# Kernel optimization log

Measured on AMD Instinct MI355X. Metric: run time of the kernel, lower is better.

## Reference

```python
import jax, jax.numpy as jnp
import numpy as np

B, S, D, H, HD = 4, 2048, 2048, 16, 128
NEG_INF = -1e10


def setup_inputs() -> dict:
    key = jax.random.key(0)
    ks = jax.random.split(key, 7)
    scale = 1.0 / np.sqrt(D)  # variance_scaling(1.0, 'fan_in') approx
    inputs_q = jax.random.normal(ks[0], (B, S, D), jnp.float32)
    inputs_kv = jax.random.normal(ks[1], (B, S, D), jnp.float32)
    mask = jax.random.randint(ks[2], (B, 1, S, S), 0, 2, jnp.int32)
    Wq = jax.random.normal(ks[3], (D, H, HD), jnp.float32) * scale
    Wk = jax.random.normal(ks[4], (D, H, HD), jnp.float32) * scale
    Wv = jax.random.normal(ks[5], (D, H, HD), jnp.float32) * scale
    Wo = jax.random.normal(ks[6], (H, HD, D), jnp.float32) * (1.0 / np.sqrt(H * HD))
    return {"inputs_q": inputs_q, "inputs_kv": inputs_kv, "mask": mask,
            "Wq": Wq, "Wk": Wk, "Wv": Wv, "Wo": Wo}


def reference(inputs_q, inputs_kv, mask, Wq, Wk, Wv, Wo):
    # QKV projections: [B,S,D] x [D,H,HD] -> [B,S,H,HD]
    q = jnp.einsum('bsd,dhk->bshk', inputs_q, Wq)
    k = jnp.einsum('bsd,dhk->bshk', inputs_kv, Wk)
    v = jnp.einsum('bsd,dhk->bshk', inputs_kv, Wv)
    # mask -> additive bias: 0 where mask>0, else -1e10
    attn_bias = jnp.where(mask > 0, 0.0, NEG_INF).astype(q.dtype)  # [B,1,S,S]
    # scaled dot-product attention
    q = q / jnp.sqrt(jnp.asarray(HD, q.dtype))
    logits = jnp.einsum('bqhd,bkhd->bhqk', q, k) + attn_bias  # [B,H,S,S]
    weights = jax.nn.softmax(logits, axis=-1)
    x = jnp.einsum('bhqk,bkhd->bqhd', weights, v)  # [B,S,H,HD]
    # out projection contracts (heads, head_dim) -> embed
    out = jnp.einsum('bqhd,hdo->bqo', x, Wo)  # [B,S,D]
    return out
```

## Files before the change

kernel.cpp:

```cpp
#include <hip/hip_runtime.h>

typedef __attribute__((ext_vector_type(4))) float f32x4;
typedef __attribute__((ext_vector_type(8))) short bf16x8;
typedef unsigned int uint;
typedef unsigned short ushort;


__device__ __forceinline__ ushort f2bf(float f) {
  union { float f; uint u; } v; v.f = f;
  uint u = v.u;
  uint r = (u + 0x7FFFu + ((u >> 16) & 1u)) >> 16;
  return (ushort)r;
}
__device__ __forceinline__ float to_f32(float f) { return f; }
__device__ __forceinline__ float to_f32(ushort u) {
  union { uint u; float f; } v; v.u = ((uint)u) << 16;
  return v.f;
}

__device__ __forceinline__ uint cvt_pk_bf16(float lo, float hi) {
  uint r;
  asm("v_cvt_pk_bf16_f32 %0, %1, %2" : "=v"(r) : "v"(lo), "v"(hi));
  return r;
}

__device__ __forceinline__ void gload_lds16(const void* g, void* l) {
  __builtin_amdgcn_global_load_lds(
      (const __attribute__((address_space(1))) void*)g,
      (__attribute__((address_space(3))) void*)l, 16, 0, 0);
}


__global__ __launch_bounds__(256)
void conv_bf16(const float* __restrict__ in, ushort* __restrict__ out, long n) {
  long i = ((long)blockIdx.x * 256 + threadIdx.x) * 8;
  if (i >= n) return;
  float4 a = *(const float4*)(in + i);
  float4 b = *(const float4*)(in + i + 4);
  union { ushort u[8]; uint4 v; } o;
  o.u[0] = f2bf(a.x); o.u[1] = f2bf(a.y); o.u[2] = f2bf(a.z); o.u[3] = f2bf(a.w);
  o.u[4] = f2bf(b.x); o.u[5] = f2bf(b.y); o.u[6] = f2bf(b.z); o.u[7] = f2bf(b.w);
  *(uint4*)(out + i) = o.v;
}

template<typename T>
__global__ __launch_bounds__(256)
void transpose_to_bf16(const T* __restrict__ in, ushort* __restrict__ out, int R, int C) {
  __shared__ float tile[32][33];
  const size_t boff = (size_t)blockIdx.z * R * C;
  in += boff; out += boff;
  const int r0 = blockIdx.y * 32, c0 = blockIdx.x * 32;
  const int x = threadIdx.x, y = threadIdx.y;
#pragma unroll
  for (int j = 0; j < 32; j += 8)
    tile[y + j][x] = to_f32(in[(size_t)(r0 + y + j) * C + c0 + x]);
  __syncthreads();
#pragma unroll
  for (int j = 0; j < 32; j += 8)
    out[(size_t)(c0 + y + j) * R + r0 + x] = f2bf(tile[x][y + j]);
}

__global__ __launch_bounds__(256)
void pack_mask(const int* __restrict__ in, uint* __restrict__ out) {
  long t = (long)blockIdx.x * 256 + threadIdx.x;
  const int4* p = (const int4*)(in + t * 32);
  uint w = 0;
#pragma unroll
  for (int i = 0; i < 8; ++i) {
    int4 v = p[i];
    w |= (v.x > 0 ? 1u : 0u) << (i * 4 + 0);
    w |= (v.y > 0 ? 1u : 0u) << (i * 4 + 1);
    w |= (v.z > 0 ? 1u : 0u) << (i * 4 + 2);
    w |= (v.w > 0 ? 1u : 0u) << (i * 4 + 3);
  }
  out[t] = w;
}


template<int OUT_BF16>
__global__ __launch_bounds__(512, 2)
void gemm256(const ushort* __restrict__ A, const ushort* __restrict__ Bt,
             void* __restrict__ C, int M, int N, int K, float scale) {
  __shared__ ushort lA[2][256 * 64];
  __shared__ ushort lB[2][256 * 64];
  const int tid = threadIdx.x;
  const int wid = tid >> 6, lane = tid & 63;
  const int lg = lane >> 4, li = lane & 15;
  const int wm = wid >> 2, wn = wid & 3;
  const int m0 = blockIdx.y * 256, n0 = blockIdx.x * 256;

  int offA[4], offB[4];
#pragma unroll
  for (int i = 0; i < 4; ++i) {
    int off = i * 8192 + tid * 16;
    int row = off >> 7;
    int col = (off & 127) ^ ((row & 7) << 4);
    offA[i] = (m0 + row) * (K * 2) + col;
    offB[i] = (n0 + row) * (K * 2) + col;
  }
  const char* Ab = (const char*)A;
  const char* Bb = (const char*)Bt;

#define STAGE256(bufi, ktb)                                                   \
  do {                                                                        \
    _Pragma("unroll") for (int i = 0; i < 4; ++i)                             \
      gload_lds16(Ab + (size_t)(offA[i] + (ktb)),                             \
                  (char*)lA[bufi] + i * 8192 + wid * 1024);                   \
    _Pragma("unroll") for (int i = 0; i < 4; ++i)                             \
      gload_lds16(Bb + (size_t)(offB[i] + (ktb)),                             \
                  (char*)lB[bufi] + i * 8192 + wid * 1024);                   \
  } while (0)

  f32x4 acc[8][4] = {};
  const int NT = K >> 6;

  STAGE256(0, 0);

  for (int t = 0; t < NT; ++t) {
    const int cur = t & 1;
    if (t > 0) __builtin_amdgcn_s_barrier();
    if (t + 1 < NT) {
      STAGE256(cur ^ 1, (t + 1) * 128);
      asm volatile("s_waitcnt vmcnt(8)" ::: "memory");
    } else {
      asm volatile("s_waitcnt vmcnt(0)" ::: "memory");
    }
    __builtin_amdgcn_s_barrier();
    __builtin_amdgcn_sched_barrier(0);

    const char* la = (const char*)lA[cur];
    const char* lb = (const char*)lB[cur];
    bf16x8 afr[4][2];
#pragma unroll
    for (int q = 0; q < 4; ++q) {
      const int mh = q >> 1;
      const int nh = (q == 1 || q == 2) ? 1 : 0;
      if ((q & 1) == 0) {
#pragma unroll
        for (int mi = 0; mi < 4; ++mi)
#pragma unroll
          for (int ks = 0; ks < 2; ++ks) {
            const int row = wm * 128 + (mh * 4 + mi) * 16 + li;
            afr[mi][ks] = *(const bf16x8*)(
                la + row * 128 + ((ks * 64 + lg * 16) ^ ((li & 7) << 4)));
          }
      }
      bf16x8 bfr[2][2];
#pragma unroll
      for (int ni = 0; ni < 2; ++ni)
#pragma unroll
        for (int ks = 0; ks < 2; ++ks) {
          const int row = wn * 64 + (nh * 2 + ni) * 16 + li;
          bfr[ni][ks] = *(const bf16x8*)(
              lb + row * 128 + ((ks * 64 + lg * 16) ^ ((li & 7) << 4)));
        }
      __builtin_amdgcn_s_setprio(1);
#pragma unroll
      for (int ks = 0; ks < 2; ++ks)
#pragma unroll
        for (int mi = 0; mi < 4; ++mi)
#pragma unroll
          for (int ni = 0; ni < 2; ++ni)
            acc[mh * 4 + mi][nh * 2 + ni] = __builtin_amdgcn_mfma_f32_16x16x32_bf16(
                afr[mi][ks], bfr[ni][ks], acc[mh * 4 + mi][nh * 2 + ni], 0, 0, 0);
      __builtin_amdgcn_s_setprio(0);
    }
  }
#undef STAGE256

  const int r0 = m0 + wm * 128 + lg * 4;
  const int c0 = n0 + wn * 64 + li;
#pragma unroll
  for (int mi = 0; mi < 8; ++mi)
#pragma unroll
    for (int ni = 0; ni < 4; ++ni)
#pragma unroll
      for (int r = 0; r < 4; ++r) {
        size_t idx = (size_t)(r0 + mi * 16 + r) * N + (c0 + ni * 16);
        float v = acc[mi][ni][r] * scale;
        if (OUT_BF16) ((ushort*)C)[idx] = f2bf(v);
        else          ((float*)C)[idx]  = v;
      }
}


__global__ __launch_bounds__(256, 2)
void flash_attn4(const ushort* __restrict__ Q, const ushort* __restrict__ K,
                 const ushort* __restrict__ VT, const uint* __restrict__ maskp,
                 ushort* __restrict__ X) {
  __shared__ ushort lK[2][64 * 128];
  __shared__ ushort lVT[2][128 * 64];
  __shared__ ushort lP[4][2][16 * 64];

  const int tid = threadIdx.x;
  const int wid = tid >> 6;
  const int lane = tid & 63;
  const int lg = lane >> 4, li = lane & 15;

  const int flat = blockIdx.x;
  const int xcd = flat & 7;
  const int j = flat >> 3;
  const int bh = xcd * 8 + (j >> 4);
  const int qt = j & 15;
  const int b = bh >> 4, h = bh & 15;
  const int q0 = qt * 128;
  const int qbase = q0 + wid * 32;

  bf16x8 bq[2][4];
#pragma unroll
  for (int g = 0; g < 2; ++g) {
    const ushort* qrow = Q + (size_t)(b * 2048 + qbase + g * 16 + li) * 2048 + h * 128;
#pragma unroll
    for (int kk = 0; kk < 4; ++kk)
      bq[g][kk] = *(const bf16x8*)(qrow + kk * 32 + lg * 8);
  }

  const uint* mqb[2] = {
      maskp + (size_t)(b * 2048 + qbase + li) * 64,
      maskp + (size_t)(b * 2048 + qbase + 16 + li) * 64};
  uint2 wcur[2] = {*(const uint2*)mqb[0], *(const uint2*)mqb[1]};

  f32x4 acc_o[2][8] = {};
  float m[2] = {-3e38f, -3e38f}, l[2] = {0.f, 0.f};

  const char* gk[4];
  const char* gv[4];
#pragma unroll
  for (int i = 0; i < 4; ++i) {
    int fl = i * 4096 + tid * 16;
    int rowK = fl >> 8;
    int colK = (fl & 255) ^ ((rowK & 15) << 4);
    gk[i] = (const char*)K + ((size_t)(b * 2048 + rowK) * 2048 + h * 128) * 2 + colK;
    int rowV = fl >> 7;
    int colV = (fl & 127) ^ ((rowV & 7) << 4);
    gv[i] = (const char*)VT + ((size_t)((b * 16 + h) * 128 + rowV) * 2048) * 2 + colV;
  }

#pragma unroll
  for (int i = 0; i < 4; ++i)
    gload_lds16(gk[i], (char*)lK[0] + i * 4096 + wid * 1024);
#pragma unroll
  for (int i = 0; i < 4; ++i)
    gload_lds16(gv[i], (char*)lVT[0] + i * 4096 + wid * 1024);
#pragma unroll
  for (int i = 0; i < 4; ++i) { gk[i] += 262144; gv[i] += 128; }
  __syncthreads();

  ushort* lp0 = lP[wid][0];
  ushort* lp1 = lP[wid][1];

  for (int it = 0; it < 32; ++it) {
    const int cur = it & 1;
    uint2 wn[2];
    if (it < 31) {
#pragma unroll
      for (int i = 0; i < 4; ++i)
        gload_lds16(gk[i], (char*)lK[cur ^ 1] + i * 4096 + wid * 1024);
#pragma unroll
      for (int i = 0; i < 4; ++i)
        gload_lds16(gv[i], (char*)lVT[cur ^ 1] + i * 4096 + wid * 1024);
#pragma unroll
      for (int i = 0; i < 4; ++i) { gk[i] += 262144; gv[i] += 128; }
      wn[0] = *(const uint2*)(mqb[0] + (it + 1) * 2);
      wn[1] = *(const uint2*)(mqb[1] + (it + 1) * 2);
    }
    const char* lk = (const char*)lK[cur];
    const char* lv = (const char*)lVT[cur];

    f32x4 accs[2][4] = {};
#pragma unroll
    for (int kk = 0; kk < 4; ++kk)
#pragma unroll
      for (int n = 0; n < 4; ++n) {
        bf16x8 ak = *(const bf16x8*)(lk + (n * 16 + li) * 256 +
                                     ((kk * 64 + lg * 16) ^ (li << 4)));
        accs[0][n] = __builtin_amdgcn_mfma_f32_16x16x32_bf16(ak, bq[0][kk], accs[0][n], 0, 0, 0);
        accs[1][n] = __builtin_amdgcn_mfma_f32_16x16x32_bf16(ak, bq[1][kk], accs[1][n], 0, 0, 0);
      }

#pragma unroll
    for (int g = 0; g < 2; ++g) {
      float sv[16];
      float pmax = -3e38f;
#pragma unroll
      for (int n = 0; n < 4; ++n) {
        uint w = (n < 2) ? wcur[g].x : wcur[g].y;
#pragma unroll
        for (int r = 0; r < 4; ++r) {
          int bit = (n & 1) * 16 + lg * 4 + r;
          float s = ((w >> bit) & 1u) ? accs[g][n][r] : -1e10f;
          sv[n * 4 + r] = s;
          pmax = fmaxf(pmax, s);
        }
      }
      pmax = fmaxf(pmax, __shfl_xor(pmax, 16, 64));
      pmax = fmaxf(pmax, __shfl_xor(pmax, 32, 64));

      if (!__all(pmax - m[g] <= 8.0f)) {
        float mnew = fmaxf(m[g], pmax);
        float alpha = __expf(m[g] - mnew);
        l[g] *= alpha;
#pragma unroll
        for (int f = 0; f < 8; ++f)
#pragma unroll
          for (int r = 0; r < 4; ++r) acc_o[g][f][r] *= alpha;
        m[g] = mnew;
      }

      float sum = 0.f;
      uint pk[8];
#pragma unroll
      for (int i = 0; i < 8; ++i) {
        float p0 = __expf(sv[2 * i] - m[g]);
        float p1 = __expf(sv[2 * i + 1] - m[g]);
        sum += p0 + p1;
        pk[i] = cvt_pk_bf16(p0, p1);
      }
      sum += __shfl_xor(sum, 16, 64);
      sum += __shfl_xor(sum, 32, 64);
      l[g] += sum;

      ushort* lpg = g ? lp1 : lp0;
#pragma unroll
      for (int n = 0; n < 4; ++n) {
        uint2 pw; pw.x = pk[2 * n]; pw.y = pk[2 * n + 1];
        *(uint2*)((char*)lpg + li * 128 + ((n * 32 + lg * 8) ^ ((li & 7) << 4))) = pw;
      }
    }

#pragma unroll
    for (int kc = 0; kc < 2; ++kc) {
      bf16x8 bp0 = *(const bf16x8*)((const char*)lp0 + li * 128 +
                                    ((kc * 64 + lg * 16) ^ ((li & 7) << 4)));
      bf16x8 bp1 = *(const bf16x8*)((const char*)lp1 + li * 128 +
                                    ((kc * 64 + lg * 16) ^ ((li & 7) << 4)));
#pragma unroll
      for (int f = 0; f < 8; ++f) {
        bf16x8 av = *(const bf16x8*)(lv + (f * 16 + li) * 128 +
                                     ((kc * 64 + lg * 16) ^ ((li & 7) << 4)));
        acc_o[0][f] = __builtin_amdgcn_mfma_f32_16x16x32_bf16(av, bp0, acc_o[0][f], 0, 0, 0);
        acc_o[1][f] = __builtin_amdgcn_mfma_f32_16x16x32_bf16(av, bp1, acc_o[1][f], 0, 0, 0);
      }
    }

    if (it < 31) { wcur[0] = wn[0]; wcur[1] = wn[1]; }
    __syncthreads();
  }

#pragma unroll
  for (int g = 0; g < 2; ++g) {
    const float inv_l = 1.0f / l[g];
    ushort* xrow = X + (size_t)(b * 2048 + qbase + g * 16 + li) * 2048 + h * 128;
#pragma unroll
    for (int f = 0; f < 8; ++f) {
      union { ushort u[4]; uint2 v; } o;
#pragma unroll
      for (int r = 0; r < 4; ++r) o.u[r] = f2bf(acc_o[g][f][r] * inv_l);
      *(uint2*)(xrow + f * 16 + lg * 4) = o.v;
    }
  }
}


extern "C" void kernel_launch(void* const* d_in, const int* in_sizes, int n_in,
                              void* d_out, int out_size, void* d_ws, size_t ws_size,
                              hipStream_t stream) {
  const float* inputs_q  = (const float*)d_in[0];
  const float* inputs_kv = (const float*)d_in[1];
  const int*   mask      = (const int*)d_in[2];
  const float* Wq        = (const float*)d_in[3];
  const float* Wk        = (const float*)d_in[4];
  const float* Wv        = (const float*)d_in[5];
  const float* Wo        = (const float*)d_in[6];
  float* out = (float*)d_out;
  char* ws = (char*)d_ws;

  uint*   maskp = (uint*)(ws + 0);
  ushort* xq    = (ushort*)(ws + 2097152);
  ushort* xkv   = (ushort*)(ws + 35651584);
  ushort* WqT   = (ushort*)(ws + 69206016);
  ushort* WkT   = (ushort*)(ws + 77594624);
  ushort* WvT   = (ushort*)(ws + 85983232);
  ushort* WoT   = (ushort*)(ws + 94371840);
  ushort* Qb    = (ushort*)(ws + 102760448);
  ushort* Kb    = (ushort*)(ws + 136314880);
  ushort* Vb    = (ushort*)(ws + 169869312);
  ushort* VTb   = xq;
  ushort* Xb    = xkv;

  const long NE = 8192L * 2048;
  conv_bf16<<<8192, 256, 0, stream>>>(inputs_q,  xq,  NE);
  conv_bf16<<<8192, 256, 0, stream>>>(inputs_kv, xkv, NE);

  dim3 tb(32, 8);
  transpose_to_bf16<float><<<dim3(64, 64, 1), tb, 0, stream>>>(Wq, WqT, 2048, 2048);
  transpose_to_bf16<float><<<dim3(64, 64, 1), tb, 0, stream>>>(Wk, WkT, 2048, 2048);
  transpose_to_bf16<float><<<dim3(64, 64, 1), tb, 0, stream>>>(Wv, WvT, 2048, 2048);
  transpose_to_bf16<float><<<dim3(64, 64, 1), tb, 0, stream>>>(Wo, WoT, 2048, 2048);

  pack_mask<<<2048, 256, 0, stream>>>(mask, maskp);

  const float qscale = 0.08838834764831845f;
  gemm256<1><<<dim3(8, 32), 512, 0, stream>>>(xq,  WqT, Qb, 8192, 2048, 2048, qscale);
  gemm256<1><<<dim3(8, 32), 512, 0, stream>>>(xkv, WkT, Kb, 8192, 2048, 2048, 1.0f);
  gemm256<1><<<dim3(8, 32), 512, 0, stream>>>(xkv, WvT, Vb, 8192, 2048, 2048, 1.0f);

  transpose_to_bf16<ushort><<<dim3(64, 64, 4), tb, 0, stream>>>(Vb, VTb, 2048, 2048);

  flash_attn4<<<1024, 256, 0, stream>>>(Qb, Kb, VTb, maskp, Xb);

  gemm256<0><<<dim3(8, 32), 512, 0, stream>>>(Xb, WoT, out, 8192, 2048, 2048, 1.0f);
}
```

Measured before the change: 601.0 us.

## Keep P in registers via 16x16x16 MFMA, base-2 exp, and split barriers

The attention kernel stops sending the probability tile through LDS. The S accumulator layout is fed straight into v_mfma_f32_16x16x16_bf16 as the B operand, and V is read as 4-element fragments. The row sum is now computed with an MFMA against a ones vector instead of shuffle reductions. The softmax uses raw v_exp_f32 (exp2), with log2(e) folded into the Q scale, and the rescale threshold is raised to match the base-2 range. The single __syncthreads is replaced by explicit vmcnt waits and split s_barriers so prefetch overlaps compute, at the cost of more, smaller MFMAs and hand-managed hazards (s_nop).

```diff
diff --git a/kernel.cpp b/kernel.cpp
--- a/kernel.cpp
+++ b/kernel.cpp
@@ -2,6 +2,7 @@
 
 typedef __attribute__((ext_vector_type(4))) float f32x4;
 typedef __attribute__((ext_vector_type(8))) short bf16x8;
+typedef __attribute__((ext_vector_type(4))) short bf16x4;
 typedef unsigned int uint;
 typedef unsigned short ushort;
 
@@ -22,6 +23,17 @@
   uint r;
   asm("v_cvt_pk_bf16_f32 %0, %1, %2" : "=v"(r) : "v"(lo), "v"(hi));
   return r;
+}
+
+__device__ __forceinline__ float fexp2(float x) {
+  float r;
+  asm("v_exp_f32 %0, %1" : "=v"(r) : "v"(x));
+  return r;
+}
+
+__device__ __forceinline__ f32x4 mfma16(bf16x4 a, bf16x4 b, f32x4 c) {
+  asm("v_mfma_f32_16x16x16_bf16 %0, %1, %2, %0" : "+v"(c) : "v"(a), "v"(b));
+  return c;
 }
 
 __device__ __forceinline__ void gload_lds16(const void* g, void* l) {
@@ -185,12 +197,11 @@
 
 
 __global__ __launch_bounds__(256, 2)
-void flash_attn4(const ushort* __restrict__ Q, const ushort* __restrict__ K,
+void flash_attn5(const ushort* __restrict__ Q, const ushort* __restrict__ K,
                  const ushort* __restrict__ VT, const uint* __restrict__ maskp,
                  ushort* __restrict__ X) {
   __shared__ ushort lK[2][64 * 128];
   __shared__ ushort lVT[2][128 * 64];
-  __shared__ ushort lP[4][2][16 * 64];
 
   const int tid = threadIdx.x;
   const int wid = tid >> 6;
@@ -221,7 +232,10 @@
   uint2 wcur[2] = {*(const uint2*)mqb[0], *(const uint2*)mqb[1]};
 
   f32x4 acc_o[2][8] = {};
-  float m[2] = {-3e38f, -3e38f}, l[2] = {0.f, 0.f};
+  f32x4 acc_l[2] = {};
+  float m[2] = {-3e38f, -3e38f};
+
+  const bf16x4 vone = {(short)0x3F80, (short)0x3F80, (short)0x3F80, (short)0x3F80};
 
   const char* gk[4];
   const char* gv[4];
@@ -236,34 +250,34 @@
     gv[i] = (const char*)VT + ((size_t)((b * 16 + h) * 128 + rowV) * 2048) * 2 + colV;
   }
 
-#pragma unroll
-  for (int i = 0; i < 4; ++i)
-    gload_lds16(gk[i], (char*)lK[0] + i * 4096 + wid * 1024);
-#pragma unroll
-  for (int i = 0; i < 4; ++i)
-    gload_lds16(gv[i], (char*)lVT[0] + i * 4096 + wid * 1024);
-#pragma unroll
-  for (int i = 0; i < 4; ++i) { gk[i] += 262144; gv[i] += 128; }
-  __syncthreads();
-
-  ushort* lp0 = lP[wid][0];
-  ushort* lp1 = lP[wid][1];
+#define FSTAGE(bufi)                                                          \
+  do {                                                                        \
+    _Pragma("unroll") for (int i = 0; i < 4; ++i)                             \
+      gload_lds16(gk[i], (char*)lK[bufi] + i * 4096 + wid * 1024);            \
+    _Pragma("unroll") for (int i = 0; i < 4; ++i)                             \
+      gload_lds16(gv[i], (char*)lVT[bufi] + i * 4096 + wid * 1024);           \
+    _Pragma("unroll") for (int i = 0; i < 4; ++i) {                           \
+      gk[i] += 262144; gv[i] += 128;                                          \
+    }                                                                         \
+  } while (0)
+
+  FSTAGE(0);
 
   for (int it = 0; it < 32; ++it) {
     const int cur = it & 1;
+    if (it > 0) __builtin_amdgcn_s_barrier();
     uint2 wn[2];
     if (it < 31) {
-#pragma unroll
-      for (int i = 0; i < 4; ++i)
-        gload_lds16(gk[i], (char*)lK[cur ^ 1] + i * 4096 + wid * 1024);
-#pragma unroll
-      for (int i = 0; i < 4; ++i)
-        gload_lds16(gv[i], (char*)lVT[cur ^ 1] + i * 4096 + wid * 1024);
-#pragma unroll
-      for (int i = 0; i < 4; ++i) { gk[i] += 262144; gv[i] += 128; }
+      FSTAGE(cur ^ 1);
       wn[0] = *(const uint2*)(mqb[0] + (it + 1) * 2);
       wn[1] = *(const uint2*)(mqb[1] + (it + 1) * 2);
-    }
+      asm volatile("s_waitcnt vmcnt(10)" ::: "memory");
+    } else {
+      asm volatile("s_waitcnt vmcnt(0)" ::: "memory");
+    }
+    __builtin_amdgcn_s_barrier();
+    __builtin_amdgcn_sched_barrier(0);
+
     const char* lk = (const char*)lK[cur];
     const char* lv = (const char*)lVT[cur];
 
@@ -278,6 +292,7 @@
         accs[1][n] = __builtin_amdgcn_mfma_f32_16x16x32_bf16(ak, bq[1][kk], accs[1][n], 0, 0, 0);
       }
 
+    uint pkg[2][8];
 #pragma unroll
     for (int g = 0; g < 2; ++g) {
       float sv[16];
@@ -296,10 +311,11 @@
       pmax = fmaxf(pmax, __shfl_xor(pmax, 16, 64));
       pmax = fmaxf(pmax, __shfl_xor(pmax, 32, 64));
 
-      if (!__all(pmax - m[g] <= 8.0f)) {
+      if (!__all(pmax - m[g] <= 11.5f)) {
         float mnew = fmaxf(m[g], pmax);
-        float alpha = __expf(m[g] - mnew);
-        l[g] *= alpha;
+        float alpha = fexp2(m[g] - mnew);
+#pragma unroll
+        for (int r = 0; r < 4; ++r) acc_l[g][r] *= alpha;
 #pragma unroll
         for (int f = 0; f < 8; ++f)
 #pragma unroll
@@ -307,49 +323,39 @@
         m[g] = mnew;
       }
 
-      float sum = 0.f;
-      uint pk[8];
 #pragma unroll
       for (int i = 0; i < 8; ++i) {
-        float p0 = __expf(sv[2 * i] - m[g]);
-        float p1 = __expf(sv[2 * i + 1] - m[g]);
-        sum += p0 + p1;
-        pk[i] = cvt_pk_bf16(p0, p1);
-      }
-      sum += __shfl_xor(sum, 16, 64);
-      sum += __shfl_xor(sum, 32, 64);
-      l[g] += sum;
-
-      ushort* lpg = g ? lp1 : lp0;
-#pragma unroll
-      for (int n = 0; n < 4; ++n) {
-        uint2 pw; pw.x = pk[2 * n]; pw.y = pk[2 * n + 1];
-        *(uint2*)((char*)lpg + li * 128 + ((n * 32 + lg * 8) ^ ((li & 7) << 4))) = pw;
-      }
-    }
-
-#pragma unroll
-    for (int kc = 0; kc < 2; ++kc) {
-      bf16x8 bp0 = *(const bf16x8*)((const char*)lp0 + li * 128 +
-                                    ((kc * 64 + lg * 16) ^ ((li & 7) << 4)));
-      bf16x8 bp1 = *(const bf16x8*)((const char*)lp1 + li * 128 +
-                                    ((kc * 64 + lg * 16) ^ ((li & 7) << 4)));
+        float p0 = fexp2(sv[2 * i] - m[g]);
+        float p1 = fexp2(sv[2 * i + 1] - m[g]);
+        pkg[g][i] = cvt_pk_bf16(p0, p1);
+      }
+    }
+
+#pragma unroll
+    for (int n = 0; n < 4; ++n) {
+      union { uint u[2]; bf16x4 v; } b0, b1;
+      b0.u[0] = pkg[0][2 * n]; b0.u[1] = pkg[0][2 * n + 1];
+      b1.u[0] = pkg[1][2 * n]; b1.u[1] = pkg[1][2 * n + 1];
+      acc_l[0] = mfma16(vone, b0.v, acc_l[0]);
+      acc_l[1] = mfma16(vone, b1.v, acc_l[1]);
 #pragma unroll
       for (int f = 0; f < 8; ++f) {
-        bf16x8 av = *(const bf16x8*)(lv + (f * 16 + li) * 128 +
-                                     ((kc * 64 + lg * 16) ^ ((li & 7) << 4)));
-        acc_o[0][f] = __builtin_amdgcn_mfma_f32_16x16x32_bf16(av, bp0, acc_o[0][f], 0, 0, 0);
-        acc_o[1][f] = __builtin_amdgcn_mfma_f32_16x16x32_bf16(av, bp1, acc_o[1][f], 0, 0, 0);
+        bf16x4 av = *(const bf16x4*)(lv + (f * 16 + li) * 128 +
+                                     ((n * 32 + lg * 8) ^ ((li & 7) << 4)));
+        acc_o[0][f] = mfma16(av, b0.v, acc_o[0][f]);
+        acc_o[1][f] = mfma16(av, b1.v, acc_o[1][f]);
       }
     }
 
     if (it < 31) { wcur[0] = wn[0]; wcur[1] = wn[1]; }
-    __syncthreads();
-  }
+  }
+#undef FSTAGE
+
+  asm volatile("s_nop 7\n\ts_nop 7\n\ts_nop 7" ::: "memory");
 
 #pragma unroll
   for (int g = 0; g < 2; ++g) {
-    const float inv_l = 1.0f / l[g];
+    const float inv_l = 1.0f / acc_l[g][0];
     ushort* xrow = X + (size_t)(b * 2048 + qbase + g * 16 + li) * 2048 + h * 128;
 #pragma unroll
     for (int f = 0; f < 8; ++f) {
@@ -400,14 +406,14 @@
 
   pack_mask<<<2048, 256, 0, stream>>>(mask, maskp);
 
-  const float qscale = 0.08838834764831845f;
+  const float qscale = 0.12751744504593677f;
   gemm256<1><<<dim3(8, 32), 512, 0, stream>>>(xq,  WqT, Qb, 8192, 2048, 2048, qscale);
   gemm256<1><<<dim3(8, 32), 512, 0, stream>>>(xkv, WkT, Kb, 8192, 2048, 2048, 1.0f);
   gemm256<1><<<dim3(8, 32), 512, 0, stream>>>(xkv, WvT, Vb, 8192, 2048, 2048, 1.0f);
 
   transpose_to_bf16<ushort><<<dim3(64, 64, 4), tb, 0, stream>>>(Vb, VTb, 2048, 2048);
 
-  flash_attn4<<<1024, 256, 0, stream>>>(Qb, Kb, VTb, maskp, Xb);
+  flash_attn5<<<1024, 256, 0, stream>>>(Qb, Kb, VTb, maskp, Xb);
 
   gemm256<0><<<dim3(8, 32), 512, 0, stream>>>(Xb, WoT, out, 8192, 2048, 2048, 1.0f);
 }
```

Result: no change. 610.5 us, median of 2 (+1.6%).
